# Performance work log

Hardware: AMD Instinct MI355X
Metric: run time of the kernel (lower is better)

Reference implementation:

```python
import jax, jax.numpy as jnp
import numpy as np

B, T, C, H, W = 1, 8, 128, 64, 64
F = 64  # num_feat


def setup_inputs() -> dict:
    key = jax.random.key(0)
    ks = jax.random.split(key, 8)
    return {
        "input1": jax.random.normal(ks[0], (B, T, C, H, W), jnp.float32),
        "input2": jax.random.normal(ks[1], (B, T, C, H, W), jnp.float32),
        "W1": jax.random.normal(ks[2], (F, C), jnp.float32) * 0.05,
        "b1": jax.random.normal(ks[3], (F,), jnp.float32) * 0.05,
        "W2": jax.random.normal(ks[4], (F, C), jnp.float32) * 0.05,
        "b2": jax.random.normal(ks[5], (F,), jnp.float32) * 0.05,
        "W3": jax.random.normal(ks[6], (F, C), jnp.float32) * 0.05,
        "b3": jax.random.normal(ks[7], (F,), jnp.float32) * 0.05,
    }


def reference(input1, input2, W1, b1, W2, b2, W3, b3):
    # act == 0 (ReLU branch). Conv1d(kernel=1) == per-position linear projection.
    b, t, c, h, w = input1.shape
    n = h * w
    x1 = input1.reshape(b, t, c, n)  # matches transpose(1,2).reshape then frame slice
    x2 = input2.reshape(b, t, c, n)
    q = jnp.einsum('fc,btcn->btnf', W1, x1) + b1          # [B,T,N,F]
    k = jnp.einsum('fc,btcn->btnf', W2, x2) + b2          # [B,T,N,F]
    g = jnp.einsum('fc,btcn->btnf', W3, x1) + b3          # [B,T,N,F]
    scores = jax.nn.relu(jnp.einsum('btnf,btmf->btnm', q, k))  # [B,T,N,N]
    out = jnp.einsum('btnm,btmf->btnf', scores, g)        # [B,T,N,F]
    # view([B,H,W,F]).permute(0,3,1,2), stacked over T -> [B,T,F,H,W]
    return out.reshape(b, t, h, w, -1).transpose(0, 1, 4, 2, 3)
```

## Files before the change

### kernel.cpp

```cpp
#include <hip/hip_runtime.h>
#include <hip/hip_bf16.h>

constexpr int T = 8;
constexpr int C = 128;
constexpr int N = 4096;
constexpr int F = 64;

typedef __bf16 bf16x8 __attribute__((ext_vector_type(8)));
typedef __bf16 bf16x4 __attribute__((ext_vector_type(4)));
typedef __bf16 bf16x2 __attribute__((ext_vector_type(2)));
typedef float  f32x4  __attribute__((ext_vector_type(4)));
typedef float  f32x16 __attribute__((ext_vector_type(16)));

__global__ __launch_bounds__(256) void setup_kernel(
    const float* __restrict__ W1, const float* __restrict__ W2,
    const float* __restrict__ W3, __bf16* __restrict__ Wb,
    float* __restrict__ out)
{
    int i = blockIdx.x * 256 + threadIdx.x;
    ((f32x4*)out)[i] = (f32x4){0.f, 0.f, 0.f, 0.f};
    if (i < 3 * F * C) {
        int p = i >> 13, r = i & 8191;
        const float* W = (p == 0) ? W1 : (p == 1) ? W2 : W3;
        Wb[i] = (__bf16)W[r];
    }
}

__global__ __launch_bounds__(256) void proj_kernel(
    const float* __restrict__ x1, const float* __restrict__ x2,
    const __bf16* __restrict__ Wb,
    const float* __restrict__ b1, const float* __restrict__ b2,
    const float* __restrict__ b3,
    __bf16* __restrict__ Qb, __bf16* __restrict__ Kb, __bf16* __restrict__ Gw)
{
    const int t  = blockIdx.x >> 6;
    const int nb = blockIdx.x & 63;
    const int n0 = nb * 64;

    constexpr int XS = 136;
    __shared__ __bf16 Xt1[64 * XS];
    __shared__ __bf16 Xt2[64 * XS];

    const int tid = threadIdx.x;
    const int ng  = tid & 15;
    const int cgi = tid >> 4;

#pragma unroll
    for (int pass = 0; pass < 2; ++pass) {
        const int c0 = cgi * 4 + pass * 64;
        const size_t base = ((size_t)t * C + c0) * (size_t)N + n0 + ng * 4;
        f32x4 v1[4], v2[4];
#pragma unroll
        for (int i = 0; i < 4; ++i) {
            v1[i] = *(const f32x4*)&x1[base + (size_t)i * N];
            v2[i] = *(const f32x4*)&x2[base + (size_t)i * N];
        }
#pragma unroll
        for (int j = 0; j < 4; ++j) {
            bf16x4 o1, o2;
#pragma unroll
            for (int i = 0; i < 4; ++i) {
                o1[i] = (__bf16)v1[i][j];
                o2[i] = (__bf16)v2[i][j];
            }
            *(bf16x4*)&Xt1[(ng * 4 + j) * XS + c0] = o1;
            *(bf16x4*)&Xt2[(ng * 4 + j) * XS + c0] = o2;
        }
    }
    __syncthreads();

    const int wave = tid >> 6, lane = tid & 63;
    const int quad = lane >> 4, l16 = lane & 15;

    bf16x8 a1[4], a2[4];
#pragma unroll
    for (int cc = 0; cc < 4; ++cc) {
        a1[cc] = *(const bf16x8*)&Xt1[(wave * 16 + l16) * XS + cc * 32 + quad * 8];
        a2[cc] = *(const bf16x8*)&Xt2[(wave * 16 + l16) * XS + cc * 32 + quad * 8];
    }

#pragma unroll
    for (int p = 0; p < 2; ++p) {
        const __bf16* W    = Wb + (size_t)p * F * C;
        const float*  bias = p ? b2 : b1;
        __bf16*       O    = p ? Kb : Qb;

        f32x4 acc[4];
#pragma unroll
        for (int ft = 0; ft < 4; ++ft) acc[ft] = (f32x4){0.f, 0.f, 0.f, 0.f};
#pragma unroll
        for (int cc = 0; cc < 4; ++cc) {
#pragma unroll
            for (int ft = 0; ft < 4; ++ft) {
                bf16x8 wf = *(const bf16x8*)&W[(ft * 16 + l16) * C + cc * 32 + quad * 8];
                bf16x8 xf = p ? a2[cc] : a1[cc];
                acc[ft] = __builtin_amdgcn_mfma_f32_16x16x32_bf16(wf, xf, acc[ft], 0, 0, 0);
            }
        }
        const int n = n0 + wave * 16 + l16;
#pragma unroll
        for (int ft = 0; ft < 4; ++ft) {
            const int f0 = ft * 16 + quad * 4;
            f32x4 bv = *(const f32x4*)&bias[f0];
            bf16x4 o;
#pragma unroll
            for (int r = 0; r < 4; ++r) o[r] = (__bf16)(acc[ft][r] + bv[r]);
            *(bf16x4*)&O[((size_t)t * N + n) * F + f0] = o;
        }
    }

    {
        const __bf16* W3b = Wb + (size_t)2 * F * C;
        f32x4 acc[4];
#pragma unroll
        for (int ft = 0; ft < 4; ++ft) acc[ft] = (f32x4){0.f, 0.f, 0.f, 0.f};
#pragma unroll
        for (int cc = 0; cc < 4; ++cc) {
#pragma unroll
            for (int ft = 0; ft < 4; ++ft) {
                bf16x8 wf = *(const bf16x8*)&W3b[(ft * 16 + l16) * C + cc * 32 + quad * 8];
                acc[ft] = __builtin_amdgcn_mfma_f32_16x16x32_bf16(a1[cc], wf, acc[ft], 0, 0, 0);
            }
        }
        const int nr0 = n0 + wave * 16 + quad * 4;
#pragma unroll
        for (int ft = 0; ft < 4; ++ft) {
            const int f = ft * 16 + l16;
            const float bv = b3[f];
            bf16x4 o;
#pragma unroll
            for (int r = 0; r < 4; ++r) o[r] = (__bf16)(acc[ft][r] + bv);
            *(bf16x4*)&Gw[((size_t)t * F + f) * (size_t)N + nr0] = o;
        }
    }
}

constexpr int KSPLIT = 4;

__global__ __launch_bounds__(256) void attn_kernel(
    const __bf16* __restrict__ Qb, const __bf16* __restrict__ Kb,
    const __bf16* __restrict__ Gw, float* __restrict__ out)
{
    const int ks = blockIdx.x & (KSPLIT - 1);
    const int qb = (blockIdx.x / KSPLIT) & 31;
    const int t  = blockIdx.x / (KSPLIT * 32);
    const int q0 = qb * 128;

    constexpr int KS = 72;
    __shared__ __bf16 Kt[64 * KS];
    __shared__ __bf16 Gt[64 * KS];

    const int tid = threadIdx.x, wave = tid >> 6, lane = tid & 63;
    const int m32 = lane & 31, hi = lane >> 5;

    bf16x8 qf[4];
    {
        const __bf16* qrow = &Qb[((size_t)t * N + q0 + wave * 32 + m32) * F + hi * 8];
#pragma unroll
        for (int fc = 0; fc < 4; ++fc)
            qf[fc] = *(const bf16x8*)(qrow + fc * 16);
    }

    f32x16 oacc[2];
#pragma unroll
    for (int ft = 0; ft < 2; ++ft)
#pragma unroll
        for (int r = 0; r < 16; ++r) oacc[ft][r] = 0.f;

    const int kb_lo = ks * (N / 64 / KSPLIT);
    const int kb_hi = kb_lo + (N / 64 / KSPLIT);

    const int r8a = tid >> 3,          c8a = (tid & 7) * 8;
    const int r8b = (tid + 256) >> 3,  c8b = c8a;

    bf16x8 kv0, kv1, gv0, gv1;
    {
        const int k0 = kb_lo * 64;
        kv0 = *(const bf16x8*)&Kb[((size_t)t * N + k0 + r8a) * F + c8a];
        kv1 = *(const bf16x8*)&Kb[((size_t)t * N + k0 + r8b) * F + c8b];
        gv0 = *(const bf16x8*)&Gw[((size_t)t * F + r8a) * (size_t)N + k0 + c8a];
        gv1 = *(const bf16x8*)&Gw[((size_t)t * F + r8b) * (size_t)N + k0 + c8b];
    }

    for (int kb = kb_lo; kb < kb_hi; ++kb) {
        __syncthreads();
        *(bf16x8*)&Kt[r8a * KS + c8a] = kv0;
        *(bf16x8*)&Kt[r8b * KS + c8b] = kv1;
        *(bf16x8*)&Gt[r8a * KS + c8a] = gv0;
        *(bf16x8*)&Gt[r8b * KS + c8b] = gv1;
        __syncthreads();

        if (kb + 1 < kb_hi) {
            const int k0 = (kb + 1) * 64;
            kv0 = *(const bf16x8*)&Kb[((size_t)t * N + k0 + r8a) * F + c8a];
            kv1 = *(const bf16x8*)&Kb[((size_t)t * N + k0 + r8b) * F + c8b];
            gv0 = *(const bf16x8*)&Gw[((size_t)t * F + r8a) * (size_t)N + k0 + c8a];
            gv1 = *(const bf16x8*)&Gw[((size_t)t * F + r8b) * (size_t)N + k0 + c8b];
        }

        bf16x8 ps[4];
#pragma unroll
        for (int kt = 0; kt < 2; ++kt) {
            f32x16 s;
#pragma unroll
            for (int r = 0; r < 16; ++r) s[r] = 0.f;
#pragma unroll
            for (int fc = 0; fc < 4; ++fc) {
                bf16x8 kf = *(const bf16x8*)&Kt[(kt * 32 + m32) * KS + fc * 16 + hi * 8];
                s = __builtin_amdgcn_mfma_f32_32x32x16_bf16(kf, qf[fc], s, 0, 0, 0);
            }
            unsigned P[8];
#pragma unroll
            for (int m = 0; m < 8; ++m) {
                union { bf16x2 h; unsigned u; } pk;
                pk.h[0] = (__bf16)fmaxf(s[2 * m], 0.f);
                pk.h[1] = (__bf16)fmaxf(s[2 * m + 1], 0.f);
                P[m] = pk.u;
            }
            asm("v_permlane32_swap_b32 %0, %1" : "+v"(P[0]), "+v"(P[2]));
            asm("v_permlane32_swap_b32 %0, %1" : "+v"(P[1]), "+v"(P[3]));
            asm("v_permlane32_swap_b32 %0, %1" : "+v"(P[4]), "+v"(P[6]));
            asm("v_permlane32_swap_b32 %0, %1" : "+v"(P[5]), "+v"(P[7]));
            union { unsigned u[4]; bf16x8 v; } lo, hiu;
            lo.u[0]  = P[0]; lo.u[1]  = P[1]; lo.u[2]  = P[2]; lo.u[3]  = P[3];
            hiu.u[0] = P[4]; hiu.u[1] = P[5]; hiu.u[2] = P[6]; hiu.u[3] = P[7];
            ps[kt * 2]     = lo.v;
            ps[kt * 2 + 1] = hiu.v;
        }

#pragma unroll
        for (int ft = 0; ft < 2; ++ft)
#pragma unroll
            for (int kt = 0; kt < 2; ++kt)
#pragma unroll
                for (int kc = 0; kc < 2; ++kc) {
                    bf16x8 gfr = *(const bf16x8*)&Gt[(ft * 32 + m32) * KS +
                                                     kt * 32 + kc * 16 + hi * 8];
                    oacc[ft] = __builtin_amdgcn_mfma_f32_32x32x16_bf16(
                        gfr, ps[kt * 2 + kc], oacc[ft], 0, 0, 0);
                }
    }

    const int q = q0 + wave * 32 + m32;
#pragma unroll
    for (int ft = 0; ft < 2; ++ft)
#pragma unroll
        for (int r = 0; r < 16; ++r) {
            int f = ft * 32 + (r & 3) + 8 * (r >> 2) + 4 * hi;
            unsafeAtomicAdd(&out[((size_t)t * F + f) * (size_t)N + q], oacc[ft][r]);
        }
}

extern "C" void kernel_launch(void* const* d_in, const int* in_sizes, int n_in,
                              void* d_out, int out_size, void* d_ws, size_t ws_size,
                              hipStream_t stream) {
    const float* x1 = (const float*)d_in[0];
    const float* x2 = (const float*)d_in[1];
    const float* W1 = (const float*)d_in[2];
    const float* b1 = (const float*)d_in[3];
    const float* W2 = (const float*)d_in[4];
    const float* b2 = (const float*)d_in[5];
    const float* W3 = (const float*)d_in[6];
    const float* b3 = (const float*)d_in[7];
    float* out = (float*)d_out;

    __bf16* Qb = (__bf16*)d_ws;
    __bf16* Kb = Qb + (size_t)T * N * F;
    __bf16* Gw = Kb + (size_t)T * N * F;
    __bf16* Wb = Gw + (size_t)T * N * F;

    setup_kernel<<<dim3(T * F * N / 4 / 256), dim3(256), 0, stream>>>(
        W1, W2, W3, Wb, out);
    proj_kernel<<<dim3(T * (N / 64)), dim3(256), 0, stream>>>(
        x1, x2, Wb, b1, b2, b3, Qb, Kb, Gw);
    attn_kernel<<<dim3(T * 32 * KSPLIT), dim3(256), 0, stream>>>(Qb, Kb, Gw, out);
}
```

Measured before the change: 151.9 us.

## Fold setup into projection kernel and double-buffer LDS tiles in attention

Removes the separate setup kernel: output zeroing and fp32-to-bf16 weight conversion now happen inside the projection kernel, saving a launch. The attention kernel now uses double-buffered shared-memory tiles for K and G, with one barrier per iteration instead of two. It also raises wave priority around the MFMA sections. The trade-offs are redundant per-block weight conversion in the projection kernel and doubled LDS usage in attention, which may lower occupancy.

```diff
diff --git a/kernel.cpp b/kernel.cpp
--- a/kernel.cpp
+++ b/kernel.cpp
@@ -12,26 +12,14 @@
 typedef float  f32x4  __attribute__((ext_vector_type(4)));
 typedef float  f32x16 __attribute__((ext_vector_type(16)));
 
-__global__ __launch_bounds__(256) void setup_kernel(
-    const float* __restrict__ W1, const float* __restrict__ W2,
-    const float* __restrict__ W3, __bf16* __restrict__ Wb,
-    float* __restrict__ out)
-{
-    int i = blockIdx.x * 256 + threadIdx.x;
-    ((f32x4*)out)[i] = (f32x4){0.f, 0.f, 0.f, 0.f};
-    if (i < 3 * F * C) {
-        int p = i >> 13, r = i & 8191;
-        const float* W = (p == 0) ? W1 : (p == 1) ? W2 : W3;
-        Wb[i] = (__bf16)W[r];
-    }
-}
-
 __global__ __launch_bounds__(256) void proj_kernel(
     const float* __restrict__ x1, const float* __restrict__ x2,
-    const __bf16* __restrict__ Wb,
+    const float* __restrict__ W1, const float* __restrict__ W2,
+    const float* __restrict__ W3,
     const float* __restrict__ b1, const float* __restrict__ b2,
     const float* __restrict__ b3,
-    __bf16* __restrict__ Qb, __bf16* __restrict__ Kb, __bf16* __restrict__ Gw)
+    __bf16* __restrict__ Qb, __bf16* __restrict__ Kb, __bf16* __restrict__ Gw,
+    float* __restrict__ out)
 {
     const int t  = blockIdx.x >> 6;
     const int nb = blockIdx.x & 63;
@@ -42,6 +30,15 @@
     __shared__ __bf16 Xt2[64 * XS];
 
     const int tid = threadIdx.x;
+
+    {
+        f32x4* o4 = (f32x4*)out;
+        const int base = blockIdx.x * 256 + tid;
+#pragma unroll
+        for (int i = 0; i < 4; ++i)
+            o4[base + i * 131072] = (f32x4){0.f, 0.f, 0.f, 0.f};
+    }
+
     const int ng  = tid & 15;
     const int cgi = tid >> 4;
 
@@ -81,9 +78,9 @@
 
 #pragma unroll
     for (int p = 0; p < 2; ++p) {
-        const __bf16* W    = Wb + (size_t)p * F * C;
-        const float*  bias = p ? b2 : b1;
-        __bf16*       O    = p ? Kb : Qb;
+        const float* W    = p ? W2 : W1;
+        const float* bias = p ? b2 : b1;
+        __bf16*      O    = p ? Kb : Qb;
 
         f32x4 acc[4];
 #pragma unroll
@@ -92,7 +89,15 @@
         for (int cc = 0; cc < 4; ++cc) {
 #pragma unroll
             for (int ft = 0; ft < 4; ++ft) {
-                bf16x8 wf = *(const bf16x8*)&W[(ft * 16 + l16) * C + cc * 32 + quad * 8];
+                const float* ws = &W[(ft * 16 + l16) * C + cc * 32 + quad * 8];
+                f32x4 w0 = *(const f32x4*)ws;
+                f32x4 w1 = *(const f32x4*)(ws + 4);
+                bf16x8 wf;
+#pragma unroll
+                for (int j = 0; j < 4; ++j) {
+                    wf[j]     = (__bf16)w0[j];
+                    wf[j + 4] = (__bf16)w1[j];
+                }
                 bf16x8 xf = p ? a2[cc] : a1[cc];
                 acc[ft] = __builtin_amdgcn_mfma_f32_16x16x32_bf16(wf, xf, acc[ft], 0, 0, 0);
             }
@@ -110,7 +115,6 @@
     }
 
     {
-        const __bf16* W3b = Wb + (size_t)2 * F * C;
         f32x4 acc[4];
 #pragma unroll
         for (int ft = 0; ft < 4; ++ft) acc[ft] = (f32x4){0.f, 0.f, 0.f, 0.f};
@@ -118,7 +122,15 @@
         for (int cc = 0; cc < 4; ++cc) {
 #pragma unroll
             for (int ft = 0; ft < 4; ++ft) {
-                bf16x8 wf = *(const bf16x8*)&W3b[(ft * 16 + l16) * C + cc * 32 + quad * 8];
+                const float* ws = &W3[(ft * 16 + l16) * C + cc * 32 + quad * 8];
+                f32x4 w0 = *(const f32x4*)ws;
+                f32x4 w1 = *(const f32x4*)(ws + 4);
+                bf16x8 wf;
+#pragma unroll
+                for (int j = 0; j < 4; ++j) {
+                    wf[j]     = (__bf16)w0[j];
+                    wf[j + 4] = (__bf16)w1[j];
+                }
                 acc[ft] = __builtin_amdgcn_mfma_f32_16x16x32_bf16(a1[cc], wf, acc[ft], 0, 0, 0);
             }
         }
@@ -147,8 +159,8 @@
     const int q0 = qb * 128;
 
     constexpr int KS = 72;
-    __shared__ __bf16 Kt[64 * KS];
-    __shared__ __bf16 Gt[64 * KS];
+    __shared__ __bf16 Kt[2][64 * KS];
+    __shared__ __bf16 Gt[2][64 * KS];
 
     const int tid = threadIdx.x, wave = tid >> 6, lane = tid & 63;
     const int m32 = lane & 31, hi = lane >> 5;
@@ -174,28 +186,40 @@
     const int r8b = (tid + 256) >> 3,  c8b = c8a;
 
     bf16x8 kv0, kv1, gv0, gv1;
+
     {
         const int k0 = kb_lo * 64;
         kv0 = *(const bf16x8*)&Kb[((size_t)t * N + k0 + r8a) * F + c8a];
         kv1 = *(const bf16x8*)&Kb[((size_t)t * N + k0 + r8b) * F + c8b];
         gv0 = *(const bf16x8*)&Gw[((size_t)t * F + r8a) * (size_t)N + k0 + c8a];
         gv1 = *(const bf16x8*)&Gw[((size_t)t * F + r8b) * (size_t)N + k0 + c8b];
-    }
+        *(bf16x8*)&Kt[0][r8a * KS + c8a] = kv0;
+        *(bf16x8*)&Kt[0][r8b * KS + c8b] = kv1;
+        *(bf16x8*)&Gt[0][r8a * KS + c8a] = gv0;
+        *(bf16x8*)&Gt[0][r8b * KS + c8b] = gv1;
+        const int k1 = k0 + 64;
+        kv0 = *(const bf16x8*)&Kb[((size_t)t * N + k1 + r8a) * F + c8a];
+        kv1 = *(const bf16x8*)&Kb[((size_t)t * N + k1 + r8b) * F + c8b];
+        gv0 = *(const bf16x8*)&Gw[((size_t)t * F + r8a) * (size_t)N + k1 + c8a];
+        gv1 = *(const bf16x8*)&Gw[((size_t)t * F + r8b) * (size_t)N + k1 + c8b];
+    }
+    __syncthreads();
 
     for (int kb = kb_lo; kb < kb_hi; ++kb) {
-        __syncthreads();
-        *(bf16x8*)&Kt[r8a * KS + c8a] = kv0;
-        *(bf16x8*)&Kt[r8b * KS + c8b] = kv1;
-        *(bf16x8*)&Gt[r8a * KS + c8a] = gv0;
-        *(bf16x8*)&Gt[r8b * KS + c8b] = gv1;
-        __syncthreads();
+        const int cur = (kb - kb_lo) & 1;
 
         if (kb + 1 < kb_hi) {
-            const int k0 = (kb + 1) * 64;
-            kv0 = *(const bf16x8*)&Kb[((size_t)t * N + k0 + r8a) * F + c8a];
-            kv1 = *(const bf16x8*)&Kb[((size_t)t * N + k0 + r8b) * F + c8b];
-            gv0 = *(const bf16x8*)&Gw[((size_t)t * F + r8a) * (size_t)N + k0 + c8a];
-            gv1 = *(const bf16x8*)&Gw[((size_t)t * F + r8b) * (size_t)N + k0 + c8b];
+            *(bf16x8*)&Kt[cur ^ 1][r8a * KS + c8a] = kv0;
+            *(bf16x8*)&Kt[cur ^ 1][r8b * KS + c8b] = kv1;
+            *(bf16x8*)&Gt[cur ^ 1][r8a * KS + c8a] = gv0;
+            *(bf16x8*)&Gt[cur ^ 1][r8b * KS + c8b] = gv1;
+            if (kb + 2 < kb_hi) {
+                const int k2 = (kb + 2) * 64;
+                kv0 = *(const bf16x8*)&Kb[((size_t)t * N + k2 + r8a) * F + c8a];
+                kv1 = *(const bf16x8*)&Kb[((size_t)t * N + k2 + r8b) * F + c8b];
+                gv0 = *(const bf16x8*)&Gw[((size_t)t * F + r8a) * (size_t)N + k2 + c8a];
+                gv1 = *(const bf16x8*)&Gw[((size_t)t * F + r8b) * (size_t)N + k2 + c8b];
+            }
         }
 
         bf16x8 ps[4];
@@ -204,11 +228,13 @@
             f32x16 s;
 #pragma unroll
             for (int r = 0; r < 16; ++r) s[r] = 0.f;
+            __builtin_amdgcn_s_setprio(1);
 #pragma unroll
             for (int fc = 0; fc < 4; ++fc) {
-                bf16x8 kf = *(const bf16x8*)&Kt[(kt * 32 + m32) * KS + fc * 16 + hi * 8];
+                bf16x8 kf = *(const bf16x8*)&Kt[cur][(kt * 32 + m32) * KS + fc * 16 + hi * 8];
                 s = __builtin_amdgcn_mfma_f32_32x32x16_bf16(kf, qf[fc], s, 0, 0, 0);
             }
+            __builtin_amdgcn_s_setprio(0);
             unsigned P[8];
 #pragma unroll
             for (int m = 0; m < 8; ++m) {
@@ -228,17 +254,21 @@
             ps[kt * 2 + 1] = hiu.v;
         }
 
+        __builtin_amdgcn_s_setprio(1);
 #pragma unroll
         for (int ft = 0; ft < 2; ++ft)
 #pragma unroll
             for (int kt = 0; kt < 2; ++kt)
 #pragma unroll
                 for (int kc = 0; kc < 2; ++kc) {
-                    bf16x8 gfr = *(const bf16x8*)&Gt[(ft * 32 + m32) * KS +
-                                                     kt * 32 + kc * 16 + hi * 8];
+                    bf16x8 gfr = *(const bf16x8*)&Gt[cur][(ft * 32 + m32) * KS +
+                                                          kt * 32 + kc * 16 + hi * 8];
                     oacc[ft] = __builtin_amdgcn_mfma_f32_32x32x16_bf16(
                         gfr, ps[kt * 2 + kc], oacc[ft], 0, 0, 0);
                 }
+        __builtin_amdgcn_s_setprio(0);
+
+        if (kb + 1 < kb_hi) __syncthreads();
     }
 
     const int q = q0 + wave * 32 + m32;
@@ -267,11 +297,8 @@
     __bf16* Qb = (__bf16*)d_ws;
     __bf16* Kb = Qb + (size_t)T * N * F;
     __bf16* Gw = Kb + (size_t)T * N * F;
-    __bf16* Wb = Gw + (size_t)T * N * F;
-
-    setup_kernel<<<dim3(T * F * N / 4 / 256), dim3(256), 0, stream>>>(
-        W1, W2, W3, Wb, out);
+
     proj_kernel<<<dim3(T * (N / 64)), dim3(256), 0, stream>>>(
-        x1, x2, Wb, b1, b2, b3, Qb, Kb, Gw);
+        x1, x2, W1, W2, W3, b1, b2, b3, Qb, Kb, Gw, out);
     attn_kernel<<<dim3(T * 32 * KSPLIT), dim3(256), 0, stream>>>(Qb, Kb, Gw, out);
 }
```

Result: slower. 164.0 us (+7.9%).

## Double query rows per wave in attention to reuse K/G tiles

Applied to the files above, without the earlier changes.

Each wave in the attention kernel now processes two 32-row query groups (256 queries per block), so every K and G fragment loaded from LDS feeds twice as many MFMAs. The grid is halved to match. s_setprio hints are placed around the MFMA chains and launch bounds now ask for 2 blocks per CU. The cost is higher register pressure from doubled accumulators and Q fragments, and only 512 blocks, which may lower occupancy or parallelism across the 256 CUs.

```diff
diff --git a/kernel.cpp b/kernel.cpp
--- a/kernel.cpp
+++ b/kernel.cpp
@@ -137,14 +137,14 @@
 
 constexpr int KSPLIT = 4;
 
-__global__ __launch_bounds__(256) void attn_kernel(
+__global__ __launch_bounds__(256, 2) void attn_kernel(
     const __bf16* __restrict__ Qb, const __bf16* __restrict__ Kb,
     const __bf16* __restrict__ Gw, float* __restrict__ out)
 {
     const int ks = blockIdx.x & (KSPLIT - 1);
-    const int qb = (blockIdx.x / KSPLIT) & 31;
-    const int t  = blockIdx.x / (KSPLIT * 32);
-    const int q0 = qb * 128;
+    const int qb = (blockIdx.x / KSPLIT) & 15;
+    const int t  = blockIdx.x / (KSPLIT * 16);
+    const int q0 = qb * 256;
 
     constexpr int KS = 72;
     __shared__ __bf16 Kt[64 * KS];
@@ -153,19 +153,23 @@
     const int tid = threadIdx.x, wave = tid >> 6, lane = tid & 63;
     const int m32 = lane & 31, hi = lane >> 5;
 
-    bf16x8 qf[4];
-    {
-        const __bf16* qrow = &Qb[((size_t)t * N + q0 + wave * 32 + m32) * F + hi * 8];
+    bf16x8 qf[2][4];
+#pragma unroll
+    for (int qg = 0; qg < 2; ++qg) {
+        const __bf16* qrow =
+            &Qb[((size_t)t * N + q0 + wave * 64 + qg * 32 + m32) * F + hi * 8];
 #pragma unroll
         for (int fc = 0; fc < 4; ++fc)
-            qf[fc] = *(const bf16x8*)(qrow + fc * 16);
-    }
-
-    f32x16 oacc[2];
-#pragma unroll
-    for (int ft = 0; ft < 2; ++ft)
-#pragma unroll
-        for (int r = 0; r < 16; ++r) oacc[ft][r] = 0.f;
+            qf[qg][fc] = *(const bf16x8*)(qrow + fc * 16);
+    }
+
+    f32x16 oacc[2][2];
+#pragma unroll
+    for (int qg = 0; qg < 2; ++qg)
+#pragma unroll
+        for (int ft = 0; ft < 2; ++ft)
+#pragma unroll
+            for (int r = 0; r < 16; ++r) oacc[qg][ft][r] = 0.f;
 
     const int kb_lo = ks * (N / 64 / KSPLIT);
     const int kb_hi = kb_lo + (N / 64 / KSPLIT);
@@ -198,36 +202,44 @@
             gv1 = *(const bf16x8*)&Gw[((size_t)t * F + r8b) * (size_t)N + k0 + c8b];
         }
 
-        bf16x8 ps[4];
+        bf16x8 ps[2][4];
 #pragma unroll
         for (int kt = 0; kt < 2; ++kt) {
-            f32x16 s;
-#pragma unroll
-            for (int r = 0; r < 16; ++r) s[r] = 0.f;
-#pragma unroll
-            for (int fc = 0; fc < 4; ++fc) {
-                bf16x8 kf = *(const bf16x8*)&Kt[(kt * 32 + m32) * KS + fc * 16 + hi * 8];
-                s = __builtin_amdgcn_mfma_f32_32x32x16_bf16(kf, qf[fc], s, 0, 0, 0);
-            }
-            unsigned P[8];
-#pragma unroll
-            for (int m = 0; m < 8; ++m) {
-                union { bf16x2 h; unsigned u; } pk;
-                pk.h[0] = (__bf16)fmaxf(s[2 * m], 0.f);
-                pk.h[1] = (__bf16)fmaxf(s[2 * m + 1], 0.f);
-                P[m] = pk.u;
-            }
-            asm("v_permlane32_swap_b32 %0, %1" : "+v"(P[0]), "+v"(P[2]));
-            asm("v_permlane32_swap_b32 %0, %1" : "+v"(P[1]), "+v"(P[3]));
-            asm("v_permlane32_swap_b32 %0, %1" : "+v"(P[4]), "+v"(P[6]));
-            asm("v_permlane32_swap_b32 %0, %1" : "+v"(P[5]), "+v"(P[7]));
-            union { unsigned u[4]; bf16x8 v; } lo, hiu;
-            lo.u[0]  = P[0]; lo.u[1]  = P[1]; lo.u[2]  = P[2]; lo.u[3]  = P[3];
-            hiu.u[0] = P[4]; hiu.u[1] = P[5]; hiu.u[2] = P[6]; hiu.u[3] = P[7];
-            ps[kt * 2]     = lo.v;
-            ps[kt * 2 + 1] = hiu.v;
-        }
-
+            bf16x8 kf[4];
+#pragma unroll
+            for (int fc = 0; fc < 4; ++fc)
+                kf[fc] = *(const bf16x8*)&Kt[(kt * 32 + m32) * KS + fc * 16 + hi * 8];
+#pragma unroll
+            for (int qg = 0; qg < 2; ++qg) {
+                f32x16 s;
+#pragma unroll
+                for (int r = 0; r < 16; ++r) s[r] = 0.f;
+                __builtin_amdgcn_s_setprio(1);
+#pragma unroll
+                for (int fc = 0; fc < 4; ++fc)
+                    s = __builtin_amdgcn_mfma_f32_32x32x16_bf16(kf[fc], qf[qg][fc], s, 0, 0, 0);
+                __builtin_amdgcn_s_setprio(0);
+                unsigned P[8];
+#pragma unroll
+                for (int m = 0; m < 8; ++m) {
+                    union { bf16x2 h; unsigned u; } pk;
+                    pk.h[0] = (__bf16)fmaxf(s[2 * m], 0.f);
+                    pk.h[1] = (__bf16)fmaxf(s[2 * m + 1], 0.f);
+                    P[m] = pk.u;
+                }
+                asm("v_permlane32_swap_b32 %0, %1" : "+v"(P[0]), "+v"(P[2]));
+                asm("v_permlane32_swap_b32 %0, %1" : "+v"(P[1]), "+v"(P[3]));
+                asm("v_permlane32_swap_b32 %0, %1" : "+v"(P[4]), "+v"(P[6]));
+                asm("v_permlane32_swap_b32 %0, %1" : "+v"(P[5]), "+v"(P[7]));
+                union { unsigned u[4]; bf16x8 v; } lo, hiu;
+                lo.u[0]  = P[0]; lo.u[1]  = P[1]; lo.u[2]  = P[2]; lo.u[3]  = P[3];
+                hiu.u[0] = P[4]; hiu.u[1] = P[5]; hiu.u[2] = P[6]; hiu.u[3] = P[7];
+                ps[qg][kt * 2]     = lo.v;
+                ps[qg][kt * 2 + 1] = hiu.v;
+            }
+        }
+
+        __builtin_amdgcn_s_setprio(1);
 #pragma unroll
         for (int ft = 0; ft < 2; ++ft)
 #pragma unroll
@@ -236,19 +248,25 @@
                 for (int kc = 0; kc < 2; ++kc) {
                     bf16x8 gfr = *(const bf16x8*)&Gt[(ft * 32 + m32) * KS +
                                                      kt * 32 + kc * 16 + hi * 8];
-                    oacc[ft] = __builtin_amdgcn_mfma_f32_32x32x16_bf16(
-                        gfr, ps[kt * 2 + kc], oacc[ft], 0, 0, 0);
+#pragma unroll
+                    for (int qg = 0; qg < 2; ++qg)
+                        oacc[qg][ft] = __builtin_amdgcn_mfma_f32_32x32x16_bf16(
+                            gfr, ps[qg][kt * 2 + kc], oacc[qg][ft], 0, 0, 0);
                 }
-    }
-
-    const int q = q0 + wave * 32 + m32;
-#pragma unroll
-    for (int ft = 0; ft < 2; ++ft)
-#pragma unroll
-        for (int r = 0; r < 16; ++r) {
-            int f = ft * 32 + (r & 3) + 8 * (r >> 2) + 4 * hi;
-            unsafeAtomicAdd(&out[((size_t)t * F + f) * (size_t)N + q], oacc[ft][r]);
-        }
+        __builtin_amdgcn_s_setprio(0);
+    }
+
+#pragma unroll
+    for (int qg = 0; qg < 2; ++qg) {
+        const int q = q0 + wave * 64 + qg * 32 + m32;
+#pragma unroll
+        for (int ft = 0; ft < 2; ++ft)
+#pragma unroll
+            for (int r = 0; r < 16; ++r) {
+                int f = ft * 32 + (r & 3) + 8 * (r >> 2) + 4 * hi;
+                unsafeAtomicAdd(&out[((size_t)t * F + f) * (size_t)N + q], oacc[qg][ft][r]);
+            }
+    }
 }
 
 extern "C" void kernel_launch(void* const* d_in, const int* in_sizes, int n_in,
@@ -273,5 +291,5 @@
         W1, W2, W3, Wb, out);
     proj_kernel<<<dim3(T * (N / 64)), dim3(256), 0, stream>>>(
         x1, x2, Wb, b1, b2, b3, Qb, Kb, Gw);
-    attn_kernel<<<dim3(T * 32 * KSPLIT), dim3(256), 0, stream>>>(Qb, Kb, Gw, out);
-}
+    attn_kernel<<<dim3(T * 16 * KSPLIT), dim3(256), 0, stream>>>(Qb, Kb, Gw, out);
+}
```

New measurement: 155.9 us. 2.6% more time.
